# Kernel tuning notes

Measured on AMD Instinct MI355X. Metric: run time of the kernel, lower is better.

The kernel has to match this reference:

```python
import jax, jax.numpy as jnp
import numpy as np

N_NODES = 50000
N_EDGES = 800000
IN_C, HID_C, OUT_C = 256, 256, 64


def _glorot(key, shape):
    fan_in, fan_out = shape[1], shape[0]
    lim = float(np.sqrt(6.0 / (fan_in + fan_out)))
    return jax.random.uniform(key, shape, jnp.float32, -lim, lim)


def setup_inputs() -> dict:
    key = jax.random.key(0)
    ks = jax.random.split(key, 8)
    x = jax.random.normal(ks[0], (N_NODES, IN_C), jnp.float32)
    edge_index = jax.random.randint(ks[1], (2, N_EDGES), 0, N_NODES, jnp.int64)
    # layer 1: SAGEConv(IN_C -> HID_C): lin_l (agg neighbors, has bias), lin_r (root, no bias)
    W_l1 = _glorot(ks[2], (HID_C, IN_C))
    b1 = jnp.zeros((HID_C,), jnp.float32)
    W_r1 = _glorot(ks[3], (HID_C, IN_C))
    # layer 2: SAGEConv(HID_C -> OUT_C)
    W_l2 = _glorot(ks[4], (OUT_C, HID_C))
    b2 = jnp.zeros((OUT_C,), jnp.float32)
    W_r2 = _glorot(ks[5], (OUT_C, HID_C))
    return {"x": x, "W_l1": W_l1, "b1": b1, "W_r1": W_r1,
            "W_l2": W_l2, "b2": b2, "W_r2": W_r2, "edge_index": edge_index}


def _sage_conv(x, src, dst, W_l, b, W_r, n_nodes):
    # mean aggregation of source-node features into destination nodes
    msg = x[src]                                               # [E, C]
    agg = jax.ops.segment_sum(msg, dst, num_segments=n_nodes)  # [N, C]
    deg = jax.ops.segment_sum(jnp.ones((src.shape[0],), x.dtype), dst,
                              num_segments=n_nodes)            # [N]
    agg = agg / jnp.maximum(deg, 1.0)[:, None]
    # out = lin_l(agg) + lin_r(x); bias only on lin_l (PyG SAGEConv default)
    return agg @ W_l.T + b + x @ W_r.T


def reference(x, W_l1, b1, W_r1, W_l2, b2, W_r2, edge_index):
    src, dst = edge_index[0], edge_index[1]
    n = x.shape[0]
    h = _sage_conv(x, src, dst, W_l1, b1, W_r1, n)
    h = jax.nn.relu(h)  # dropout is identity in eval mode
    out = _sage_conv(h, src, dst, W_l2, b2, W_r2, n)
    return out
```

## Files before the change

### kernel.cpp

```cpp
#include <hip/hip_runtime.h>

#define IN_C 256
#define HID_C 256
#define OUT_C 64

#define NBK 64
#define NPAD 50176
#define N2 (NPAD / 2)
#define NCH (NPAD / 256)

typedef __attribute__((ext_vector_type(8))) short bf16x8;
typedef __attribute__((ext_vector_type(4))) float f32x4;
typedef __attribute__((ext_vector_type(2))) float f32x2;
typedef __attribute__((ext_vector_type(8))) unsigned short ushortx8;
typedef __attribute__((ext_vector_type(4))) unsigned int u32x4;
typedef __attribute__((ext_vector_type(2))) unsigned int u32x2;

__device__ inline float b2f(unsigned short u) {
    union { unsigned int u; float f; } v; v.u = ((unsigned int)u) << 16; return v.f;
}
__device__ inline unsigned short f2b(float f) {
    union { float f; unsigned int u; } v; v.f = f;
    unsigned int u = v.u;
    unsigned int r = (u + 0x7fffu + ((u >> 16) & 1u)) >> 16;
    return (unsigned short)r;
}

__device__ __forceinline__ unsigned char f2fp8(float v) {
    int pk = __builtin_amdgcn_cvt_pk_fp8_f32(v, v, 0, false);
    return (unsigned char)(pk & 0xff);
}
__device__ __forceinline__ void fp8acc4(unsigned int w, float& a0, float& a1, float& a2, float& a3) {
    f32x2 lo = __builtin_amdgcn_cvt_pk_f32_fp8((int)w, false);
    f32x2 hi = __builtin_amdgcn_cvt_pk_f32_fp8((int)w, true);
    a0 += lo.x; a1 += lo.y; a2 += hi.x; a3 += hi.y;
}

__device__ __forceinline__ void gl2lds16(const ushort* g, ushort* l) {
    __builtin_amdgcn_global_load_lds((const __attribute__((address_space(1))) void*)g,
                                     (__attribute__((address_space(3))) void*)l, 16, 0, 0);
}

__device__ __forceinline__ void conv8(const float* __restrict__ src, ushort* __restrict__ dst, int u) {
    const float4* p = (const float4*)(src + (size_t)u * 8);
    float4 a = p[0], b = p[1];
    ushort4 o0 = make_ushort4(f2b(a.x), f2b(a.y), f2b(a.z), f2b(a.w));
    ushort4 o1 = make_ushort4(f2b(b.x), f2b(b.y), f2b(b.z), f2b(b.w));
    ((ushort4*)(dst + (size_t)u * 8))[0] = o0;
    ((ushort4*)(dst + (size_t)u * 8))[1] = o1;
}


__global__ __launch_bounds__(1024) void k_front(const int* __restrict__ dst, int E, int EPB,
                                                ushort* __restrict__ rank,
                                                unsigned int* __restrict__ cnt32,
                                                int* __restrict__ chunkpart,
                                                const float* __restrict__ x, ushort* __restrict__ xb,
                                                int xUnits,
                                                const float* __restrict__ Wl1, const float* __restrict__ Wr1,
                                                const float* __restrict__ Wl2, const float* __restrict__ Wr2,
                                                ushort* __restrict__ Wc1, ushort* __restrict__ Wc2) {
    const int bid = blockIdx.x;
    const int t = threadIdx.x;

    if (bid < NBK) {
        __shared__ unsigned int h[N2];
        for (int i = t; i < N2; i += 1024) h[i] = 0;
        __syncthreads();

        const int e0 = bid * EPB;
        const int e1 = min(e0 + EPB, E);
        for (int e = e0 + t; e < e1; e += 1024) {
            int d = dst[e];
            int sh = (d & 1) << 4;
            unsigned int old = atomicAdd(&h[d >> 1], 1u << sh);
            rank[e] = (ushort)((old >> sh) & 0xffffu);
        }
        __syncthreads();

        unsigned int* outp = cnt32 + (size_t)bid * N2;
        for (int i = t; i < N2; i += 1024) outp[i] = h[i];

        if (t < NCH) {
            int c = t;
            int sum = 0;
#pragma unroll 8
            for (int j = 0; j < 128; ++j) {
                unsigned int v = h[c * 128 + ((j + c) & 127)];
                sum += (int)(v & 0xffffu) + (int)(v >> 16);
            }
            chunkpart[c * NBK + bid] = sum;
        }
        return;
    }

    const int ct = (bid - NBK) * 1024 + t;
    const int cn = 256 * 1024;
    for (int i = ct; i < 20480; i += cn) {
        if (i < 8192)       conv8(Wl1, Wc1,         i);
        else if (i < 16384) conv8(Wr1, Wc1 + 65536, i - 8192);
        else if (i < 18432) conv8(Wl2, Wc2,         i - 16384);
        else                conv8(Wr2, Wc2 + 16384, i - 18432);
    }
    for (int u = ct; u < xUnits; u += cn) conv8(x, xb, u);
}


__global__ __launch_bounds__(256) void k_scan(const unsigned int* __restrict__ cnt32,
                                              const int* __restrict__ chunkpart, int N,
                                              int* __restrict__ row_start,
                                              ushort* __restrict__ off16) {
    __shared__ int s[256];
    const int bid = blockIdx.x;
    const int t = threadIdx.x;

    int pre = 0;
    const int limit = bid * NBK;
    for (int i = t; i < limit; i += 256) pre += chunkpart[i];
    s[t] = pre;
    __syncthreads();
    for (int o = 128; o > 0; o >>= 1) {
        if (t < o) s[t] += s[t + o];
        __syncthreads();
    }
    const int chunk_off = s[0];
    __syncthreads();

    const int i = bid * 256 + t;
    const ushort* cnt16 = (const ushort*)cnt32;
    int run = 0;
#pragma unroll 8
    for (int b = 0; b < NBK; ++b) {
        ushort cv = cnt16[(size_t)b * NPAD + i];
        off16[(size_t)b * NPAD + i] = (ushort)run;
        run += cv;
    }
    int deg = run;

    s[t] = deg;
    __syncthreads();
    for (int o = 1; o < 256; o <<= 1) {
        int xx = (t >= o) ? s[t - o] : 0;
        __syncthreads();
        s[t] += xx;
        __syncthreads();
    }
    if (i < N) row_start[i + 1] = s[t] + chunk_off;
    if (i == 0) row_start[0] = 0;
}


__global__ __launch_bounds__(256) void k_gemm_l1(const ushort* __restrict__ A,
                                                 const ushort* __restrict__ W,
                                                 unsigned char* __restrict__ Cp,
                                                 ushort* __restrict__ Cr,
                                                 int N, int nScat,
                                                 const int* __restrict__ src, const int* __restrict__ dst,
                                                 const ushort* __restrict__ rank,
                                                 const int* __restrict__ row_start,
                                                 const ushort* __restrict__ off16,
                                                 int E, int EPB, int* __restrict__ eidx) {
    if (blockIdx.x < (unsigned)nScat) {
        int base = blockIdx.x * 256 + threadIdx.x;
        int stride = nScat * 256;
        for (int e = base; e < E; e += stride) {
            int d = dst[e];
            int b = e / EPB;
            eidx[row_start[d] + (int)off16[(size_t)b * NPAD + d] + (int)rank[e]] = src[e];
        }
        return;
    }

    __shared__ ushort Aall[64 * 256];
    __shared__ ushort Wb[2 * 128 * 64];

    const int bx = blockIdx.x - nScat;
    const int t = threadIdx.x;
    const int bm = bx * 64;

    const int wid  = t >> 6;
    const int lane = t & 63;
    const int wr = wid >> 1;
    const int wc = wid & 1;
    const int lr = lane & 15;
    const int lk = lane >> 4;

    {
        const int arow7 = (t >> 5) & 7;
        const int asrc  = ((t & 31) ^ arow7) << 3;
#pragma unroll
        for (int i = 0; i < 8; ++i) {
            gl2lds16(A + (size_t)(bm + i * 8 + (t >> 5)) * 256 + asrc,
                     Aall + i * 2048 + t * 8);
        }
        const int wrow7 = (t >> 3) & 7;
        const int wsrc  = ((t & 7) ^ wrow7) << 3;
#pragma unroll
        for (int i = 0; i < 4; ++i) {
            gl2lds16(W + (size_t)(i * 32 + (t >> 3)) * 256 + 0 + wsrc,
                     Wb + i * 2048 + t * 8);
        }
    }
    __syncthreads();

    f32x4 acc[2][4];
    int s = 0;
#pragma unroll
    for (int by = 0; by < 4; ++by) {
#pragma unroll
        for (int m = 0; m < 2; ++m)
#pragma unroll
            for (int n = 0; n < 4; ++n) acc[m][n] = (f32x4){0.f, 0.f, 0.f, 0.f};

#pragma unroll
        for (int kk = 0; kk < 4; ++kk, ++s) {
            const int sn = s + 1;
            if (sn < 16) {
                const int by_n = sn >> 2, kk_n = sn & 3, buf_n = sn & 1;
                const int wrow7 = (t >> 3) & 7;
                const int wsrc  = ((t & 7) ^ wrow7) << 3;
#pragma unroll
                for (int i = 0; i < 4; ++i) {
                    gl2lds16(W + (size_t)(by_n * 128 + i * 32 + (t >> 3)) * 256 + kk_n * 64 + wsrc,
                             Wb + buf_n * 8192 + i * 2048 + t * 8);
                }
            }

            const int kb = kk * 8;
            const int buf = s & 1;
            const int sw = lr & 7;
#pragma unroll
            for (int ks = 0; ks < 2; ++ks) {
                bf16x8 a[2], b[4];
                const int ck = ks * 4 + lk;
#pragma unroll
                for (int m = 0; m < 2; ++m)
                    a[m] = *(const bf16x8*)(Aall + (wr * 32 + m * 16 + lr) * 256 + ((kb + (ck ^ sw)) << 3));
#pragma unroll
                for (int n = 0; n < 4; ++n)
                    b[n] = *(const bf16x8*)(Wb + buf * 8192 + (wc * 64 + n * 16 + lr) * 64 + ((ck ^ sw) << 3));
#pragma unroll
                for (int m = 0; m < 2; ++m)
#pragma unroll
                    for (int n = 0; n < 4; ++n)
                        acc[m][n] = __builtin_amdgcn_mfma_f32_16x16x32_bf16(a[m], b[n], acc[m][n], 0, 0, 0);
            }

            if (kk == 3) {
                const bool isP = (by * 128 + wc * 64) < HID_C;
#pragma unroll
                for (int m = 0; m < 2; ++m)
#pragma unroll
                    for (int r2 = 0; r2 < 4; ++r2) {
                        int row = bm + wr * 32 + m * 16 + lk * 4 + r2;
                        if (row < N) {
                            if (isP) {
#pragma unroll
                                for (int n = 0; n < 4; ++n) {
                                    int col = by * 128 + wc * 64 + n * 16 + lr;
                                    Cp[(size_t)row * HID_C + col] = f2fp8(acc[m][n][r2]);
                                }
                            } else {
#pragma unroll
                                for (int n = 0; n < 4; ++n) {
                                    int col = by * 128 + wc * 64 + n * 16 + lr - HID_C;
                                    Cr[(size_t)row * HID_C + col] = f2b(acc[m][n][r2]);
                                }
                            }
                        }
                    }
            }
            __syncthreads();
        }
    }
}


__global__ __launch_bounds__(256) void k_gemm_mfma(const ushort* __restrict__ A,
                                                   const ushort* __restrict__ W,
                                                   unsigned char* __restrict__ Cp,
                                                   ushort* __restrict__ Cr,
                                                   int N, int K, int PC, int nby, int nwg) {
    __shared__ ushort As[2][128 * 64];
    __shared__ ushort Bs[2][128 * 64];

    const int orig = blockIdx.x;
    const int q = nwg >> 3, r = nwg & 7;
    const int xcd = orig & 7;
    const int base = (xcd < r) ? xcd * (q + 1) : r * (q + 1) + (xcd - r) * q;
    const int wgid = base + (orig >> 3);
    const int bx = wgid / nby, by = wgid % nby;

    const int wid  = threadIdx.x >> 6;
    const int lane = threadIdx.x & 63;
    const int wr = wid >> 1, wc = wid & 1;
    const int bm = bx * 128;
    const int bn = by * 128;
    const int lr = lane & 15;
    const int lk = lane >> 4;
    const int srow   = lane >> 3;
    const int schunk = lane & 7;

    f32x4 acc[4][4];
#pragma unroll
    for (int m = 0; m < 4; ++m)
#pragma unroll
        for (int n = 0; n < 4; ++n) acc[m][n] = (f32x4){0.f, 0.f, 0.f, 0.f};

#pragma unroll
    for (int i = 0; i < 4; ++i) {
        int seg = wid * 4 + i;
        int row = seg * 8 + srow;
        gl2lds16(A + (size_t)(bm + row) * K + schunk * 8, As[0] + seg * 512);
        gl2lds16(W + (size_t)(bn + row) * K + schunk * 8, Bs[0] + seg * 512);
    }
    __syncthreads();

    int cur = 0;
    for (int k0 = 0; k0 < K; k0 += 64) {
        const int kn = k0 + 64;
        if (kn < K) {
#pragma unroll
            for (int i = 0; i < 4; ++i) {
                int seg = wid * 4 + i;
                int row = seg * 8 + srow;
                gl2lds16(A + (size_t)(bm + row) * K + kn + schunk * 8, As[cur ^ 1] + seg * 512);
                gl2lds16(W + (size_t)(bn + row) * K + kn + schunk * 8, Bs[cur ^ 1] + seg * 512);
            }
        }

#pragma unroll
        for (int ks = 0; ks < 2; ++ks) {
            bf16x8 a[4], b[4];
#pragma unroll
            for (int m = 0; m < 4; ++m)
                a[m] = *(const bf16x8*)(As[cur] + (wr * 64 + m * 16 + lr) * 64 + ks * 32 + lk * 8);
#pragma unroll
            for (int n = 0; n < 4; ++n)
                b[n] = *(const bf16x8*)(Bs[cur] + (wc * 64 + n * 16 + lr) * 64 + ks * 32 + lk * 8);
#pragma unroll
            for (int m = 0; m < 4; ++m)
#pragma unroll
                for (int n = 0; n < 4; ++n)
                    acc[m][n] = __builtin_amdgcn_mfma_f32_16x16x32_bf16(a[m], b[n], acc[m][n], 0, 0, 0);
        }
        __syncthreads();
        cur ^= 1;
    }

    const bool isP = (bn + wc * 64) < PC;
#pragma unroll
    for (int m = 0; m < 4; ++m)
#pragma unroll
        for (int r2 = 0; r2 < 4; ++r2) {
            int row = bm + wr * 64 + m * 16 + lk * 4 + r2;
            if (row < N) {
                if (isP) {
#pragma unroll
                    for (int n = 0; n < 4; ++n) {
                        int col = bn + wc * 64 + n * 16 + lr;
                        Cp[(size_t)row * PC + col] = f2fp8(acc[m][n][r2]);
                    }
                } else {
#pragma unroll
                    for (int n = 0; n < 4; ++n) {
                        int col = bn + wc * 64 + n * 16 + lr - PC;
                        Cr[(size_t)row * PC + col] = f2b(acc[m][n][r2]);
                    }
                }
            }
        }
}


__global__ __launch_bounds__(256) void k_agg1(const unsigned char* __restrict__ P1,
                                              const ushort* __restrict__ R1,
                                              const float* __restrict__ bias,
                                              const int* __restrict__ row_start,
                                              const int* __restrict__ eidx,
                                              ushort* __restrict__ h, int N) {
    int node = (blockIdx.x * blockDim.x + threadIdx.x) >> 6;
    int lane = threadIdx.x & 63;
    if (node >= N) return;
    const int slot = lane >> 4;
    const int sub  = lane & 15;
    int s0 = row_start[node], s1 = row_start[node + 1];

    float acc[16];
#pragma unroll
    for (int i = 0; i < 16; ++i) acc[i] = 0.f;

    for (int e = s0 + slot; e < s1; e += 16) {
        int e1 = e + 4, e2 = e + 8, e3 = e + 12;
        bool h1 = e1 < s1, h2 = e2 < s1, h3 = e3 < s1;
        int sA = eidx[e];
        int sB = h1 ? eidx[e1] : sA;
        int sC = h2 ? eidx[e2] : sA;
        int sD = h3 ? eidx[e3] : sA;
        u32x4 a = *(const u32x4*)(P1 + (size_t)sA * 256 + sub * 16);
        u32x4 b = *(const u32x4*)(P1 + (size_t)sB * 256 + sub * 16);
        u32x4 c = *(const u32x4*)(P1 + (size_t)sC * 256 + sub * 16);
        u32x4 d = *(const u32x4*)(P1 + (size_t)sD * 256 + sub * 16);
#pragma unroll
        for (int w = 0; w < 4; ++w) fp8acc4(a[w], acc[w*4], acc[w*4+1], acc[w*4+2], acc[w*4+3]);
        if (h1) {
#pragma unroll
            for (int w = 0; w < 4; ++w) fp8acc4(b[w], acc[w*4], acc[w*4+1], acc[w*4+2], acc[w*4+3]);
        }
        if (h2) {
#pragma unroll
            for (int w = 0; w < 4; ++w) fp8acc4(c[w], acc[w*4], acc[w*4+1], acc[w*4+2], acc[w*4+3]);
        }
        if (h3) {
#pragma unroll
            for (int w = 0; w < 4; ++w) fp8acc4(d[w], acc[w*4], acc[w*4+1], acc[w*4+2], acc[w*4+3]);
        }
    }

#pragma unroll
    for (int i = 0; i < 16; ++i) {
        acc[i] += __shfl_xor(acc[i], 16, 64);
        acc[i] += __shfl_xor(acc[i], 32, 64);
    }

    if (slot == 0) {
        int d = s1 - s0;
        float inv = 1.0f / (float)(d > 1 ? d : 1);
        const ushort* rp = R1 + (size_t)node * 256 + sub * 16;
        ushortx8 r0 = *(const ushortx8*)(rp);
        ushortx8 r1 = *(const ushortx8*)(rp + 8);
        const float* bp = bias + sub * 16;
        ushortx8 o0, o1;
#pragma unroll
        for (int i = 0; i < 8; ++i) {
            float v0 = fmaxf(acc[i] * inv + bp[i] + b2f(r0[i]), 0.f);
            float v1 = fmaxf(acc[i + 8] * inv + bp[i + 8] + b2f(r1[i]), 0.f);
            o0[i] = f2b(v0);
            o1[i] = f2b(v1);
        }
        ushort* hp = h + (size_t)node * 256 + sub * 16;
        *(ushortx8*)(hp) = o0;
        *(ushortx8*)(hp + 8) = o1;
    }
}


__global__ __launch_bounds__(256) void k_agg2(const unsigned char* __restrict__ P2,
                                              const ushort* __restrict__ R2,
                                              const float* __restrict__ bias,
                                              const int* __restrict__ row_start,
                                              const int* __restrict__ eidx,
                                              float* __restrict__ out, int N) {
    int node = (blockIdx.x * blockDim.x + threadIdx.x) >> 6;
    int lane = threadIdx.x & 63;
    if (node >= N) return;
    const int slot = lane >> 3;
    const int sub  = lane & 7;
    int s0 = row_start[node], s1 = row_start[node + 1];

    float acc[8];
#pragma unroll
    for (int i = 0; i < 8; ++i) acc[i] = 0.f;

    for (int e = s0 + slot; e < s1; e += 32) {
        int e1 = e + 8, e2 = e + 16, e3 = e + 24;
        bool h1 = e1 < s1, h2 = e2 < s1, h3 = e3 < s1;
        int sA = eidx[e];
        int sB = h1 ? eidx[e1] : sA;
        int sC = h2 ? eidx[e2] : sA;
        int sD = h3 ? eidx[e3] : sA;
        u32x2 a = *(const u32x2*)(P2 + (size_t)sA * 64 + sub * 8);
        u32x2 b = *(const u32x2*)(P2 + (size_t)sB * 64 + sub * 8);
        u32x2 c = *(const u32x2*)(P2 + (size_t)sC * 64 + sub * 8);
        u32x2 d = *(const u32x2*)(P2 + (size_t)sD * 64 + sub * 8);
#pragma unroll
        for (int w = 0; w < 2; ++w) fp8acc4(a[w], acc[w*4], acc[w*4+1], acc[w*4+2], acc[w*4+3]);
        if (h1) {
#pragma unroll
            for (int w = 0; w < 2; ++w) fp8acc4(b[w], acc[w*4], acc[w*4+1], acc[w*4+2], acc[w*4+3]);
        }
        if (h2) {
#pragma unroll
            for (int w = 0; w < 2; ++w) fp8acc4(c[w], acc[w*4], acc[w*4+1], acc[w*4+2], acc[w*4+3]);
        }
        if (h3) {
#pragma unroll
            for (int w = 0; w < 2; ++w) fp8acc4(d[w], acc[w*4], acc[w*4+1], acc[w*4+2], acc[w*4+3]);
        }
    }

#pragma unroll
    for (int i = 0; i < 8; ++i) {
        acc[i] += __shfl_xor(acc[i], 8, 64);
        acc[i] += __shfl_xor(acc[i], 16, 64);
        acc[i] += __shfl_xor(acc[i], 32, 64);
    }

    if (slot == 0) {
        int d = s1 - s0;
        float inv = 1.0f / (float)(d > 1 ? d : 1);
        ushortx8 rv = *(const ushortx8*)(R2 + (size_t)node * 64 + sub * 8);
        const float* bp = bias + sub * 8;
        float o[8];
#pragma unroll
        for (int i = 0; i < 8; ++i) o[i] = acc[i] * inv + bp[i] + b2f(rv[i]);
        float4* op = (float4*)(out + (size_t)node * 64 + sub * 8);
        op[0] = make_float4(o[0], o[1], o[2], o[3]);
        op[1] = make_float4(o[4], o[5], o[6], o[7]);
    }
}


extern "C" void kernel_launch(void* const* d_in, const int* in_sizes, int n_in,
                              void* d_out, int out_size, void* d_ws, size_t ws_size,
                              hipStream_t stream) {
    const float* x    = (const float*)d_in[0];
    const float* W_l1 = (const float*)d_in[1];
    const float* b1   = (const float*)d_in[2];
    const float* W_r1 = (const float*)d_in[3];
    const float* W_l2 = (const float*)d_in[4];
    const float* b2   = (const float*)d_in[5];
    const float* W_r2 = (const float*)d_in[6];
    const int*   ei   = (const int*)d_in[7];

    const int N = in_sizes[0] / IN_C;
    const int E = in_sizes[7] / 2;
    const int EPB = (E + NBK - 1) / NBK;
    const int* src = ei;
    const int* dst = ei + E;

    char* ws = (char*)d_ws;
    size_t off_ = 0;
    auto alloc = [&](size_t bytes) -> void* {
        void* p = ws + off_;
        off_ += (bytes + 255) & ~(size_t)255;
        return p;
    };
    unsigned int*  cnt32     = (unsigned int*)alloc((size_t)NBK * N2 * 4);
    ushort*        off16     = (ushort*)alloc((size_t)NBK * NPAD * 2);
    int*           chunkpart = (int*)alloc((size_t)NCH * NBK * 4);
    int*           row_start = (int*)alloc((size_t)(N + 1) * 4);
    ushort*        rank      = (ushort*)alloc((size_t)E * 2);
    int*           eidx      = (int*)alloc((size_t)E * 4);
    ushort*        xb        = (ushort*)alloc((size_t)N * IN_C * 2);
    ushort*        Wc1       = (ushort*)alloc((size_t)2 * HID_C * IN_C * 2);
    ushort*        Wc2       = (ushort*)alloc((size_t)2 * OUT_C * HID_C * 2);
    unsigned char* P1        = (unsigned char*)alloc((size_t)N * HID_C);
    ushort*        R1        = (ushort*)alloc((size_t)N * HID_C * 2);
    ushort*        h         = (ushort*)alloc((size_t)N * HID_C * 2);
    unsigned char* P2        = (unsigned char*)alloc((size_t)N * OUT_C);
    ushort*        R2        = (ushort*)alloc((size_t)N * OUT_C * 2);
    (void)alloc(128 * 512 * 2);
    (void)ws_size; (void)n_in; (void)out_size;

    {
        int xUnits = N * IN_C / 8;
        k_front<<<NBK + 256, 1024, 0, stream>>>(dst, E, EPB, rank, cnt32, chunkpart,
                                                x, xb, xUnits,
                                                W_l1, W_r1, W_l2, W_r2, Wc1, Wc2);
    }

    k_scan<<<NCH, 256, 0, stream>>>(cnt32, chunkpart, N, row_start, off16);

    {
        const int nScat = 448;
        int nbx = (N + 63) / 64;
        k_gemm_l1<<<nScat + nbx, 256, 0, stream>>>(xb, Wc1, P1, R1, N,
                                                   nScat, src, dst, rank, row_start, off16,
                                                   E, EPB, eidx);
        k_agg1<<<(N + 3) / 4, 256, 0, stream>>>(P1, R1, b1, row_start, eidx, h, N);
    }

    {
        int nbx = (N + 127) / 128, nby = (2 * OUT_C) / 128;
        int nwg = nbx * nby;
        k_gemm_mfma<<<nwg, 256, 0, stream>>>(h, Wc2, P2, R2, N, HID_C, OUT_C, nby, nwg);
        k_agg2<<<(N + 3) / 4, 256, 0, stream>>>(P2, R2, b2, row_start, eidx, (float*)d_out, N);
    }
}
```

Baseline: 147.7 us.

## Fuse fp32-to-bf16 conversion of x into layer-1 GEMM tile load

Removes the separate pass in the front kernel that converted all of x to bf16 in global memory. The layer-1 GEMM now reads fp32 rows of x directly, converts them in registers, and writes them into swizzled LDS, which drops a full write plus re-read of the bf16 copy of x. The edge-scatter blocks also change from a grid-stride loop to contiguous per-block edge ranges. The cost is synchronous fp32 loads (twice the bytes per tile) instead of async global-to-LDS copies, plus heavier register use in the GEMM prologue.

```diff
diff --git a/kernel.cpp b/kernel.cpp
--- a/kernel.cpp
+++ b/kernel.cpp
@@ -55,8 +55,6 @@
                                                 ushort* __restrict__ rank,
                                                 unsigned int* __restrict__ cnt32,
                                                 int* __restrict__ chunkpart,
-                                                const float* __restrict__ x, ushort* __restrict__ xb,
-                                                int xUnits,
                                                 const float* __restrict__ Wl1, const float* __restrict__ Wr1,
                                                 const float* __restrict__ Wl2, const float* __restrict__ Wr2,
                                                 ushort* __restrict__ Wc1, ushort* __restrict__ Wc2) {
@@ -94,15 +92,13 @@
         return;
     }
 
-    const int ct = (bid - NBK) * 1024 + t;
-    const int cn = 256 * 1024;
-    for (int i = ct; i < 20480; i += cn) {
+    const int i = (bid - NBK) * 1024 + t;
+    if (i < 20480) {
         if (i < 8192)       conv8(Wl1, Wc1,         i);
         else if (i < 16384) conv8(Wr1, Wc1 + 65536, i - 8192);
         else if (i < 18432) conv8(Wl2, Wc2,         i - 16384);
         else                conv8(Wr2, Wc2 + 16384, i - 18432);
     }
-    for (int u = ct; u < xUnits; u += cn) conv8(x, xb, u);
 }
 
 
@@ -150,7 +146,7 @@
 }
 
 
-__global__ __launch_bounds__(256) void k_gemm_l1(const ushort* __restrict__ A,
+__global__ __launch_bounds__(256) void k_gemm_l1(const float* __restrict__ x,
                                                  const ushort* __restrict__ W,
                                                  unsigned char* __restrict__ Cp,
                                                  ushort* __restrict__ Cr,
@@ -159,11 +155,11 @@
                                                  const ushort* __restrict__ rank,
                                                  const int* __restrict__ row_start,
                                                  const ushort* __restrict__ off16,
-                                                 int E, int EPB, int* __restrict__ eidx) {
+                                                 int E, int EPB, int per, int* __restrict__ eidx) {
     if (blockIdx.x < (unsigned)nScat) {
-        int base = blockIdx.x * 256 + threadIdx.x;
-        int stride = nScat * 256;
-        for (int e = base; e < E; e += stride) {
+        const int e0 = blockIdx.x * per;
+        const int e1 = min(e0 + per, E);
+        for (int e = e0 + (int)threadIdx.x; e < e1; e += 256) {
             int d = dst[e];
             int b = e / EPB;
             eidx[row_start[d] + (int)off16[(size_t)b * NPAD + d] + (int)rank[e]] = src[e];
@@ -186,12 +182,27 @@
     const int lk = lane >> 4;
 
     {
-        const int arow7 = (t >> 5) & 7;
-        const int asrc  = ((t & 31) ^ arow7) << 3;
-#pragma unroll
-        for (int i = 0; i < 8; ++i) {
-            gl2lds16(A + (size_t)(bm + i * 8 + (t >> 5)) * 256 + asrc,
-                     Aall + i * 2048 + t * 8);
+        const int r4  = t >> 2;
+        const int cg  = t & 3;
+        const int row = bm + r4;
+        const float4* xp = (const float4*)(x + (size_t)row * 256 + cg * 64);
+        float4 v[16];
+        if (row < N) {
+#pragma unroll
+            for (int j = 0; j < 16; ++j) v[j] = xp[j];
+        } else {
+#pragma unroll
+            for (int j = 0; j < 16; ++j) v[j] = make_float4(0.f, 0.f, 0.f, 0.f);
+        }
+        const int r7 = r4 & 7;
+#pragma unroll
+        for (int j = 0; j < 8; ++j) {
+            float4 a = v[2 * j], b = v[2 * j + 1];
+            ushort4 o0 = make_ushort4(f2b(a.x), f2b(a.y), f2b(a.z), f2b(a.w));
+            ushort4 o1 = make_ushort4(f2b(b.x), f2b(b.y), f2b(b.z), f2b(b.w));
+            ushort* dp = Aall + r4 * 256 + (cg * 8 + (j ^ r7)) * 8;
+            ((ushort4*)dp)[0] = o0;
+            ((ushort4*)dp)[1] = o1;
         }
         const int wrow7 = (t >> 3) & 7;
         const int wsrc  = ((t & 7) ^ wrow7) << 3;
@@ -542,7 +553,6 @@
     int*           row_start = (int*)alloc((size_t)(N + 1) * 4);
     ushort*        rank      = (ushort*)alloc((size_t)E * 2);
     int*           eidx      = (int*)alloc((size_t)E * 4);
-    ushort*        xb        = (ushort*)alloc((size_t)N * IN_C * 2);
     ushort*        Wc1       = (ushort*)alloc((size_t)2 * HID_C * IN_C * 2);
     ushort*        Wc2       = (ushort*)alloc((size_t)2 * OUT_C * HID_C * 2);
     unsigned char* P1        = (unsigned char*)alloc((size_t)N * HID_C);
@@ -553,21 +563,18 @@
     (void)alloc(128 * 512 * 2);
     (void)ws_size; (void)n_in; (void)out_size;
 
-    {
-        int xUnits = N * IN_C / 8;
-        k_front<<<NBK + 256, 1024, 0, stream>>>(dst, E, EPB, rank, cnt32, chunkpart,
-                                                x, xb, xUnits,
-                                                W_l1, W_r1, W_l2, W_r2, Wc1, Wc2);
-    }
+    k_front<<<NBK + 32, 1024, 0, stream>>>(dst, E, EPB, rank, cnt32, chunkpart,
+                                           W_l1, W_r1, W_l2, W_r2, Wc1, Wc2);
 
     k_scan<<<NCH, 256, 0, stream>>>(cnt32, chunkpart, N, row_start, off16);
 
     {
         const int nScat = 448;
-        int nbx = (N + 63) / 64;
-        k_gemm_l1<<<nScat + nbx, 256, 0, stream>>>(xb, Wc1, P1, R1, N,
-                                                   nScat, src, dst, rank, row_start, off16,
-                                                   E, EPB, eidx);
+        const int per = (E + nScat - 1) / nScat;
+        const int nbx = (N + 63) / 64;
+        k_gemm_l1<<<nScat + nbx, 256, 0, stream>>>(x, Wc1, P1, R1, N, nScat,
+                                                   src, dst, rank, row_start, off16,
+                                                   E, EPB, per, eidx);
         k_agg1<<<(N + 3) / 4, 256, 0, stream>>>(P1, R1, b1, row_start, eidx, h, N);
     }
 
```

Result: no change. 148.3 us (+0.4%).

## Pack degree histogram into 8-bit counters, double histogram blocks, chunk edge scatter

Applied to the files above, without the earlier changes.

The per-block destination histogram now packs four 8-bit counters per LDS word instead of two 16-bit ones. That halves the LDS footprint and lets twice as many blocks (128) share the edge-counting work. Per-edge ranks shrink to one byte, and the edge-index scatter now gives each block a contiguous range of edges instead of a grid stride, to improve locality on the per-block offset table. The trade-off is that the scan kernel now walks and writes twice as many per-block offsets. Counts also silently overflow if any node gets more than 255 edges within one block's edge chunk.

```diff
diff --git a/kernel.cpp b/kernel.cpp
--- a/kernel.cpp
+++ b/kernel.cpp
@@ -4,9 +4,9 @@
 #define HID_C 256
 #define OUT_C 64
 
-#define NBK 64
+#define NBK 128
 #define NPAD 50176
-#define N2 (NPAD / 2)
+#define N4 (NPAD / 4)
 #define NCH (NPAD / 256)
 
 typedef __attribute__((ext_vector_type(8))) short bf16x8;
@@ -52,7 +52,7 @@
 
 
 __global__ __launch_bounds__(1024) void k_front(const int* __restrict__ dst, int E, int EPB,
-                                                ushort* __restrict__ rank,
+                                                unsigned char* __restrict__ rank,
                                                 unsigned int* __restrict__ cnt32,
                                                 int* __restrict__ chunkpart,
                                                 const float* __restrict__ x, ushort* __restrict__ xb,
@@ -64,30 +64,31 @@
     const int t = threadIdx.x;
 
     if (bid < NBK) {
-        __shared__ unsigned int h[N2];
-        for (int i = t; i < N2; i += 1024) h[i] = 0;
+        __shared__ unsigned int h[N4];
+        for (int i = t; i < N4; i += 1024) h[i] = 0;
         __syncthreads();
 
         const int e0 = bid * EPB;
         const int e1 = min(e0 + EPB, E);
         for (int e = e0 + t; e < e1; e += 1024) {
             int d = dst[e];
-            int sh = (d & 1) << 4;
-            unsigned int old = atomicAdd(&h[d >> 1], 1u << sh);
-            rank[e] = (ushort)((old >> sh) & 0xffffu);
+            int sh = (d & 3) << 3;
+            unsigned int old = atomicAdd(&h[d >> 2], 1u << sh);
+            rank[e] = (unsigned char)((old >> sh) & 0xffu);
         }
         __syncthreads();
 
-        unsigned int* outp = cnt32 + (size_t)bid * N2;
-        for (int i = t; i < N2; i += 1024) outp[i] = h[i];
+        unsigned int* outp = cnt32 + (size_t)bid * N4;
+        for (int i = t; i < N4; i += 1024) outp[i] = h[i];
 
         if (t < NCH) {
             int c = t;
             int sum = 0;
 #pragma unroll 8
-            for (int j = 0; j < 128; ++j) {
-                unsigned int v = h[c * 128 + ((j + c) & 127)];
-                sum += (int)(v & 0xffffu) + (int)(v >> 16);
+            for (int j = 0; j < 64; ++j) {
+                unsigned int v = h[c * 64 + ((j + c) & 63)];
+                sum += (int)(v & 0xffu) + (int)((v >> 8) & 0xffu)
+                     + (int)((v >> 16) & 0xffu) + (int)(v >> 24);
             }
             chunkpart[c * NBK + bid] = sum;
         }
@@ -127,11 +128,11 @@
     __syncthreads();
 
     const int i = bid * 256 + t;
-    const ushort* cnt16 = (const ushort*)cnt32;
+    const unsigned char* cnt8 = (const unsigned char*)cnt32;
     int run = 0;
 #pragma unroll 8
     for (int b = 0; b < NBK; ++b) {
-        ushort cv = cnt16[(size_t)b * NPAD + i];
+        unsigned char cv = cnt8[(size_t)b * NPAD + i];
         off16[(size_t)b * NPAD + i] = (ushort)run;
         run += cv;
     }
@@ -156,14 +157,14 @@
                                                  ushort* __restrict__ Cr,
                                                  int N, int nScat,
                                                  const int* __restrict__ src, const int* __restrict__ dst,
-                                                 const ushort* __restrict__ rank,
+                                                 const unsigned char* __restrict__ rank,
                                                  const int* __restrict__ row_start,
                                                  const ushort* __restrict__ off16,
-                                                 int E, int EPB, int* __restrict__ eidx) {
+                                                 int E, int EPB, int per, int* __restrict__ eidx) {
     if (blockIdx.x < (unsigned)nScat) {
-        int base = blockIdx.x * 256 + threadIdx.x;
-        int stride = nScat * 256;
-        for (int e = base; e < E; e += stride) {
+        const int e0 = blockIdx.x * per;
+        const int e1 = min(e0 + per, E);
+        for (int e = e0 + (int)threadIdx.x; e < e1; e += 256) {
             int d = dst[e];
             int b = e / EPB;
             eidx[row_start[d] + (int)off16[(size_t)b * NPAD + d] + (int)rank[e]] = src[e];
@@ -536,11 +537,11 @@
         off_ += (bytes + 255) & ~(size_t)255;
         return p;
     };
-    unsigned int*  cnt32     = (unsigned int*)alloc((size_t)NBK * N2 * 4);
+    unsigned int*  cnt32     = (unsigned int*)alloc((size_t)NBK * N4 * 4);
     ushort*        off16     = (ushort*)alloc((size_t)NBK * NPAD * 2);
     int*           chunkpart = (int*)alloc((size_t)NCH * NBK * 4);
     int*           row_start = (int*)alloc((size_t)(N + 1) * 4);
-    ushort*        rank      = (ushort*)alloc((size_t)E * 2);
+    unsigned char* rank      = (unsigned char*)alloc((size_t)E);
     int*           eidx      = (int*)alloc((size_t)E * 4);
     ushort*        xb        = (ushort*)alloc((size_t)N * IN_C * 2);
     ushort*        Wc1       = (ushort*)alloc((size_t)2 * HID_C * IN_C * 2);
@@ -564,10 +565,11 @@
 
     {
         const int nScat = 448;
-        int nbx = (N + 63) / 64;
-        k_gemm_l1<<<nScat + nbx, 256, 0, stream>>>(xb, Wc1, P1, R1, N,
-                                                   nScat, src, dst, rank, row_start, off16,
-                                                   E, EPB, eidx);
+        const int per = (E + nScat - 1) / nScat;
+        const int nbx = (N + 63) / 64;
+        k_gemm_l1<<<nScat + nbx, 256, 0, stream>>>(xb, Wc1, P1, R1, N, nScat,
+                                                   src, dst, rank, row_start, off16,
+                                                   E, EPB, per, eidx);
         k_agg1<<<(N + 3) / 4, 256, 0, stream>>>(P1, R1, b1, row_start, eidx, h, N);
     }
 
```

After: 159.8 us. 1.08x slower.

## Fuse layer-1 aggregation with layer-2 GEMM via LDS-resident h tile

Applied to the files above, without the earlier changes.

Merges the layer-1 neighbor aggregation (mean plus bias, root term and ReLU) with the layer-2 projection GEMM. Each 64-node block builds its bf16 h tile in swizzled LDS and immediately multiplies it by the double-buffered layer-2 weights with MFMA. This removes the h buffer write and read and one kernel launch. It also changes the scatter blocks in k_gemm_l1 from a grid-stride loop to contiguous edge ranges per block. The trade-off is that the fused kernel has fewer, heavier blocks (784) that use more LDS, which can lower occupancy and latency hiding for the gather phase.

```diff
diff --git a/kernel.cpp b/kernel.cpp
--- a/kernel.cpp
+++ b/kernel.cpp
@@ -159,11 +159,11 @@
                                                  const ushort* __restrict__ rank,
                                                  const int* __restrict__ row_start,
                                                  const ushort* __restrict__ off16,
-                                                 int E, int EPB, int* __restrict__ eidx) {
+                                                 int E, int EPB, int per, int* __restrict__ eidx) {
     if (blockIdx.x < (unsigned)nScat) {
-        int base = blockIdx.x * 256 + threadIdx.x;
-        int stride = nScat * 256;
-        for (int e = base; e < E; e += stride) {
+        const int e0 = blockIdx.x * per;
+        const int e1 = min(e0 + per, E);
+        for (int e = e0 + (int)threadIdx.x; e < e1; e += 256) {
             int d = dst[e];
             int b = e / EPB;
             eidx[row_start[d] + (int)off16[(size_t)b * NPAD + d] + (int)rank[e]] = src[e];
@@ -276,172 +276,164 @@
 }
 
 
-__global__ __launch_bounds__(256) void k_gemm_mfma(const ushort* __restrict__ A,
-                                                   const ushort* __restrict__ W,
-                                                   unsigned char* __restrict__ Cp,
-                                                   ushort* __restrict__ Cr,
-                                                   int N, int K, int PC, int nby, int nwg) {
-    __shared__ ushort As[2][128 * 64];
-    __shared__ ushort Bs[2][128 * 64];
+__global__ __launch_bounds__(256) void k_agg1_l2(const unsigned char* __restrict__ P1,
+                                                 const ushort* __restrict__ R1,
+                                                 const float* __restrict__ bias,
+                                                 const int* __restrict__ row_start,
+                                                 const int* __restrict__ eidx,
+                                                 const ushort* __restrict__ W,
+                                                 unsigned char* __restrict__ P2,
+                                                 ushort* __restrict__ R2, int N) {
+    __shared__ ushort Aall[64 * 256];
+    __shared__ ushort Wb[2 * 128 * 64];
 
     const int orig = blockIdx.x;
-    const int q = nwg >> 3, r = nwg & 7;
-    const int xcd = orig & 7;
-    const int base = (xcd < r) ? xcd * (q + 1) : r * (q + 1) + (xcd - r) * q;
-    const int wgid = base + (orig >> 3);
-    const int bx = wgid / nby, by = wgid % nby;
-
-    const int wid  = threadIdx.x >> 6;
-    const int lane = threadIdx.x & 63;
+    const int bx = (orig & 7) * 98 + (orig >> 3);
+    const int bm = bx * 64;
+    const int t = threadIdx.x;
+    const int wid = t >> 6, lane = t & 63;
+
+    {
+        const int wrow7 = (t >> 3) & 7;
+        const int wsrc  = ((t & 7) ^ wrow7) << 3;
+#pragma unroll
+        for (int i = 0; i < 4; ++i)
+            gl2lds16(W + (size_t)(i * 32 + (t >> 3)) * 256 + wsrc, Wb + i * 2048 + t * 8);
+    }
+
+    {
+        const int slot = lane >> 4;
+        const int sub  = lane & 15;
+        for (int nl = wid * 16; nl < wid * 16 + 16; ++nl) {
+            const int node = bm + nl;
+            if (node >= N) continue;
+            int s0 = row_start[node], s1 = row_start[node + 1];
+
+            float acc[16];
+#pragma unroll
+            for (int i = 0; i < 16; ++i) acc[i] = 0.f;
+
+            for (int e = s0 + slot; e < s1; e += 16) {
+                int e1 = e + 4, e2 = e + 8, e3 = e + 12;
+                bool h1 = e1 < s1, h2 = e2 < s1, h3 = e3 < s1;
+                int sA = eidx[e];
+                int sB = h1 ? eidx[e1] : sA;
+                int sC = h2 ? eidx[e2] : sA;
+                int sD = h3 ? eidx[e3] : sA;
+                u32x4 a = *(const u32x4*)(P1 + (size_t)sA * 256 + sub * 16);
+                u32x4 b = *(const u32x4*)(P1 + (size_t)sB * 256 + sub * 16);
+                u32x4 c = *(const u32x4*)(P1 + (size_t)sC * 256 + sub * 16);
+                u32x4 d = *(const u32x4*)(P1 + (size_t)sD * 256 + sub * 16);
+#pragma unroll
+                for (int w = 0; w < 4; ++w) fp8acc4(a[w], acc[w*4], acc[w*4+1], acc[w*4+2], acc[w*4+3]);
+                if (h1) {
+#pragma unroll
+                    for (int w = 0; w < 4; ++w) fp8acc4(b[w], acc[w*4], acc[w*4+1], acc[w*4+2], acc[w*4+3]);
+                }
+                if (h2) {
+#pragma unroll
+                    for (int w = 0; w < 4; ++w) fp8acc4(c[w], acc[w*4], acc[w*4+1], acc[w*4+2], acc[w*4+3]);
+                }
+                if (h3) {
+#pragma unroll
+                    for (int w = 0; w < 4; ++w) fp8acc4(d[w], acc[w*4], acc[w*4+1], acc[w*4+2], acc[w*4+3]);
+                }
+            }
+
+#pragma unroll
+            for (int i = 0; i < 16; ++i) {
+                acc[i] += __shfl_xor(acc[i], 16, 64);
+                acc[i] += __shfl_xor(acc[i], 32, 64);
+            }
+
+            if (slot == 0) {
+                int d = s1 - s0;
+                float inv = 1.0f / (float)(d > 1 ? d : 1);
+                const ushort* rp = R1 + (size_t)node * 256 + sub * 16;
+                ushortx8 r0 = *(const ushortx8*)(rp);
+                ushortx8 r1 = *(const ushortx8*)(rp + 8);
+                const float* bp = bias + sub * 16;
+                ushortx8 o0, o1;
+#pragma unroll
+                for (int i = 0; i < 8; ++i) {
+                    float v0 = fmaxf(acc[i] * inv + bp[i] + b2f(r0[i]), 0.f);
+                    float v1 = fmaxf(acc[i + 8] * inv + bp[i + 8] + b2f(r1[i]), 0.f);
+                    o0[i] = f2b(v0);
+                    o1[i] = f2b(v1);
+                }
+                const int r7 = nl & 7;
+                const int c0 = 2 * sub, c1 = c0 + 1;
+                *(ushortx8*)(Aall + nl * 256 + (((c0 & ~7) | ((c0 & 7) ^ r7)) << 3)) = o0;
+                *(ushortx8*)(Aall + nl * 256 + (((c1 & ~7) | ((c1 & 7) ^ r7)) << 3)) = o1;
+            }
+        }
+    }
+    __syncthreads();
+
     const int wr = wid >> 1, wc = wid & 1;
-    const int bm = bx * 128;
-    const int bn = by * 128;
-    const int lr = lane & 15;
-    const int lk = lane >> 4;
-    const int srow   = lane >> 3;
-    const int schunk = lane & 7;
-
-    f32x4 acc[4][4];
-#pragma unroll
-    for (int m = 0; m < 4; ++m)
-#pragma unroll
-        for (int n = 0; n < 4; ++n) acc[m][n] = (f32x4){0.f, 0.f, 0.f, 0.f};
-
-#pragma unroll
-    for (int i = 0; i < 4; ++i) {
-        int seg = wid * 4 + i;
-        int row = seg * 8 + srow;
-        gl2lds16(A + (size_t)(bm + row) * K + schunk * 8, As[0] + seg * 512);
-        gl2lds16(W + (size_t)(bn + row) * K + schunk * 8, Bs[0] + seg * 512);
-    }
-    __syncthreads();
-
-    int cur = 0;
-    for (int k0 = 0; k0 < K; k0 += 64) {
-        const int kn = k0 + 64;
-        if (kn < K) {
-#pragma unroll
-            for (int i = 0; i < 4; ++i) {
-                int seg = wid * 4 + i;
-                int row = seg * 8 + srow;
-                gl2lds16(A + (size_t)(bm + row) * K + kn + schunk * 8, As[cur ^ 1] + seg * 512);
-                gl2lds16(W + (size_t)(bn + row) * K + kn + schunk * 8, Bs[cur ^ 1] + seg * 512);
-            }
-        }
-
+    const int lr = lane & 15, lk = lane >> 4;
+
+    f32x4 acc2[2][4];
+#pragma unroll
+    for (int m = 0; m < 2; ++m)
+#pragma unroll
+        for (int n = 0; n < 4; ++n) acc2[m][n] = (f32x4){0.f, 0.f, 0.f, 0.f};
+
+#pragma unroll
+    for (int kk = 0; kk < 4; ++kk) {
+        const int sn = kk + 1;
+        if (sn < 4) {
+            const int wrow7 = (t >> 3) & 7;
+            const int wsrc  = ((t & 7) ^ wrow7) << 3;
+#pragma unroll
+            for (int i = 0; i < 4; ++i)
+                gl2lds16(W + (size_t)(i * 32 + (t >> 3)) * 256 + sn * 64 + wsrc,
+                         Wb + (sn & 1) * 8192 + i * 2048 + t * 8);
+        }
+
+        const int buf = kk & 1;
+        const int sw = lr & 7;
 #pragma unroll
         for (int ks = 0; ks < 2; ++ks) {
-            bf16x8 a[4], b[4];
-#pragma unroll
-            for (int m = 0; m < 4; ++m)
-                a[m] = *(const bf16x8*)(As[cur] + (wr * 64 + m * 16 + lr) * 64 + ks * 32 + lk * 8);
+            const int ck = ks * 4 + lk;
+            bf16x8 a[2], b[4];
+#pragma unroll
+            for (int m = 0; m < 2; ++m)
+                a[m] = *(const bf16x8*)(Aall + (wr * 32 + m * 16 + lr) * 256 + ((kk * 8 + (ck ^ sw)) << 3));
 #pragma unroll
             for (int n = 0; n < 4; ++n)
-                b[n] = *(const bf16x8*)(Bs[cur] + (wc * 64 + n * 16 + lr) * 64 + ks * 32 + lk * 8);
-#pragma unroll
-            for (int m = 0; m < 4; ++m)
+                b[n] = *(const bf16x8*)(Wb + buf * 8192 + (wc * 64 + n * 16 + lr) * 64 + ((ck ^ sw) << 3));
+#pragma unroll
+            for (int m = 0; m < 2; ++m)
 #pragma unroll
                 for (int n = 0; n < 4; ++n)
-                    acc[m][n] = __builtin_amdgcn_mfma_f32_16x16x32_bf16(a[m], b[n], acc[m][n], 0, 0, 0);
+                    acc2[m][n] = __builtin_amdgcn_mfma_f32_16x16x32_bf16(a[m], b[n], acc2[m][n], 0, 0, 0);
         }
         __syncthreads();
-        cur ^= 1;
-    }
-
-    const bool isP = (bn + wc * 64) < PC;
-#pragma unroll
-    for (int m = 0; m < 4; ++m)
+    }
+
+    const bool isP = (wc == 0);
+#pragma unroll
+    for (int m = 0; m < 2; ++m)
 #pragma unroll
         for (int r2 = 0; r2 < 4; ++r2) {
-            int row = bm + wr * 64 + m * 16 + lk * 4 + r2;
+            int row = bm + wr * 32 + m * 16 + lk * 4 + r2;
             if (row < N) {
                 if (isP) {
 #pragma unroll
                     for (int n = 0; n < 4; ++n) {
-                        int col = bn + wc * 64 + n * 16 + lr;
-                        Cp[(size_t)row * PC + col] = f2fp8(acc[m][n][r2]);
+                        int col = n * 16 + lr;
+                        P2[(size_t)row * OUT_C + col] = f2fp8(acc2[m][n][r2]);
                     }
                 } else {
 #pragma unroll
                     for (int n = 0; n < 4; ++n) {
-                        int col = bn + wc * 64 + n * 16 + lr - PC;
-                        Cr[(size_t)row * PC + col] = f2b(acc[m][n][r2]);
+                        int col = n * 16 + lr;
+                        R2[(size_t)row * OUT_C + col] = f2b(acc2[m][n][r2]);
                     }
                 }
             }
         }
-}
-
-
-__global__ __launch_bounds__(256) void k_agg1(const unsigned char* __restrict__ P1,
-                                              const ushort* __restrict__ R1,
-                                              const float* __restrict__ bias,
-                                              const int* __restrict__ row_start,
-                                              const int* __restrict__ eidx,
-                                              ushort* __restrict__ h, int N) {
-    int node = (blockIdx.x * blockDim.x + threadIdx.x) >> 6;
-    int lane = threadIdx.x & 63;
-    if (node >= N) return;
-    const int slot = lane >> 4;
-    const int sub  = lane & 15;
-    int s0 = row_start[node], s1 = row_start[node + 1];
-
-    float acc[16];
-#pragma unroll
-    for (int i = 0; i < 16; ++i) acc[i] = 0.f;
-
-    for (int e = s0 + slot; e < s1; e += 16) {
-        int e1 = e + 4, e2 = e + 8, e3 = e + 12;
-        bool h1 = e1 < s1, h2 = e2 < s1, h3 = e3 < s1;
-        int sA = eidx[e];
-        int sB = h1 ? eidx[e1] : sA;
-        int sC = h2 ? eidx[e2] : sA;
-        int sD = h3 ? eidx[e3] : sA;
-        u32x4 a = *(const u32x4*)(P1 + (size_t)sA * 256 + sub * 16);
-        u32x4 b = *(const u32x4*)(P1 + (size_t)sB * 256 + sub * 16);
-        u32x4 c = *(const u32x4*)(P1 + (size_t)sC * 256 + sub * 16);
-        u32x4 d = *(const u32x4*)(P1 + (size_t)sD * 256 + sub * 16);
-#pragma unroll
-        for (int w = 0; w < 4; ++w) fp8acc4(a[w], acc[w*4], acc[w*4+1], acc[w*4+2], acc[w*4+3]);
-        if (h1) {
-#pragma unroll
-            for (int w = 0; w < 4; ++w) fp8acc4(b[w], acc[w*4], acc[w*4+1], acc[w*4+2], acc[w*4+3]);
-        }
-        if (h2) {
-#pragma unroll
-            for (int w = 0; w < 4; ++w) fp8acc4(c[w], acc[w*4], acc[w*4+1], acc[w*4+2], acc[w*4+3]);
-        }
-        if (h3) {
-#pragma unroll
-            for (int w = 0; w < 4; ++w) fp8acc4(d[w], acc[w*4], acc[w*4+1], acc[w*4+2], acc[w*4+3]);
-        }
-    }
-
-#pragma unroll
-    for (int i = 0; i < 16; ++i) {
-        acc[i] += __shfl_xor(acc[i], 16, 64);
-        acc[i] += __shfl_xor(acc[i], 32, 64);
-    }
-
-    if (slot == 0) {
-        int d = s1 - s0;
-        float inv = 1.0f / (float)(d > 1 ? d : 1);
-        const ushort* rp = R1 + (size_t)node * 256 + sub * 16;
-        ushortx8 r0 = *(const ushortx8*)(rp);
-        ushortx8 r1 = *(const ushortx8*)(rp + 8);
-        const float* bp = bias + sub * 16;
-        ushortx8 o0, o1;
-#pragma unroll
-        for (int i = 0; i < 8; ++i) {
-            float v0 = fmaxf(acc[i] * inv + bp[i] + b2f(r0[i]), 0.f);
-            float v1 = fmaxf(acc[i + 8] * inv + bp[i + 8] + b2f(r1[i]), 0.f);
-            o0[i] = f2b(v0);
-            o1[i] = f2b(v1);
-        }
-        ushort* hp = h + (size_t)node * 256 + sub * 16;
-        *(ushortx8*)(hp) = o0;
-        *(ushortx8*)(hp + 8) = o1;
-    }
 }
 
 
@@ -547,7 +539,6 @@
     ushort*        Wc2       = (ushort*)alloc((size_t)2 * OUT_C * HID_C * 2);
     unsigned char* P1        = (unsigned char*)alloc((size_t)N * HID_C);
     ushort*        R1        = (ushort*)alloc((size_t)N * HID_C * 2);
-    ushort*        h         = (ushort*)alloc((size_t)N * HID_C * 2);
     unsigned char* P2        = (unsigned char*)alloc((size_t)N * OUT_C);
     ushort*        R2        = (ushort*)alloc((size_t)N * OUT_C * 2);
     (void)alloc(128 * 512 * 2);
@@ -564,17 +555,14 @@
 
     {
         const int nScat = 448;
-        int nbx = (N + 63) / 64;
-        k_gemm_l1<<<nScat + nbx, 256, 0, stream>>>(xb, Wc1, P1, R1, N,
-                                                   nScat, src, dst, rank, row_start, off16,
-                                                   E, EPB, eidx);
-        k_agg1<<<(N + 3) / 4, 256, 0, stream>>>(P1, R1, b1, row_start, eidx, h, N);
-    }
-
-    {
-        int nbx = (N + 127) / 128, nby = (2 * OUT_C) / 128;
-        int nwg = nbx * nby;
-        k_gemm_mfma<<<nwg, 256, 0, stream>>>(h, Wc2, P2, R2, N, HID_C, OUT_C, nby, nwg);
-        k_agg2<<<(N + 3) / 4, 256, 0, stream>>>(P2, R2, b2, row_start, eidx, (float*)d_out, N);
-    }
-}
+        const int per = (E + nScat - 1) / nScat;
+        const int nbx = (N + 63) / 64;
+        k_gemm_l1<<<nScat + nbx, 256, 0, stream>>>(xb, Wc1, P1, R1, N, nScat,
+                                                   src, dst, rank, row_start, off16,
+                                                   E, EPB, per, eidx);
+        k_agg1_l2<<<NPAD / 64, 256, 0, stream>>>(P1, R1, b1, row_start, eidx,
+                                                 Wc2, P2, R2, N);
+    }
+
+    k_agg2<<<(N + 3) / 4, 256, 0, stream>>>(P2, R2, b2, row_start, eidx, (float*)d_out, N);
+}
```

After: 200.3 us. +35.6%, slower.
